# Optimization experiments

Hardware: AMD Instinct MI355X
Metric: run time of the kernel (lower is better)

Reference implementation:

```python
import jax, jax.numpy as jnp
import numpy as np

B, CIN, COUT, T, K = 8, 64, 64, 16384, 127


def setup_inputs() -> dict:
    key = jax.random.key(0)
    kx, kw = jax.random.split(key)
    x = jax.random.normal(kx, (B, CIN, T), dtype=jnp.float32)
    sigma = np.sqrt(2.0 / (CIN * K + COUT)).astype(np.float32)
    W = jax.random.normal(kw, (COUT, CIN, K), dtype=jnp.float32) * sigma
    return {"x": x, "W": W}


def reference(x, W):
    # Full linear convolution via FFT (true convolution, matches
    # torchaudio.functional.fftconvolve), summed over in_channels,
    # then trimmed to mode='same' (output length == T, centered).
    T_ = x.shape[-1]
    K_ = W.shape[-1]
    n = T_ + K_ - 1  # linear-conv length, no circular wraparound
    Xf = jnp.fft.rfft(x, n=n)   # [B, Cin, nf] complex
    Wf = jnp.fft.rfft(W, n=n)   # [Cout, Cin, nf] complex
    # Batched complex multiply-accumulate over in_channels (single pass,
    # no per-output-channel redundant FFTs).
    Yf = jnp.einsum('bif,oif->bof', Xf, Wf)  # [B, Cout, nf]
    y_full = jnp.fft.irfft(Yf, n=n)          # [B, Cout, T+K-1]
    start = (K_ - 1) // 2                    # 'same': centered crop
    return y_full[..., start:start + T_]
```

## Files before the change

kernel.cpp:

```cpp
#include <hip/hip_runtime.h>

#define T_LEN 16384
#define CIN   64
#define COUT  64
#define KTAPS 127
#define TN    512
#define XROWS 640
#define XPITCH_B 144
#define WT_KS 4096

typedef __attribute__((ext_vector_type(8)))  __bf16 bf16x8;
typedef __attribute__((ext_vector_type(16))) float  f32x16;
typedef __attribute__((ext_vector_type(4)))  float  float4v;

__device__ inline unsigned short f2bf(float f) {
    unsigned u = __builtin_bit_cast(unsigned, f);
    u += 0x7fffu + ((u >> 16) & 1u);
    return (unsigned short)(u >> 16);
}

__global__ void wt_transform(const float* __restrict__ W,
                             unsigned short* __restrict__ Wt) {
    int t  = blockIdx.x * 256 + threadIdx.x;
    int kp = t >> 9, c = t & 511;
    int f = c >> 6, kg = (c >> 5) & 1, l31 = c & 31;
    int cc = f >> 1, m = f & 1;
    int o = m * 32 + l31, ib = cc * 16 + kg * 8;
    const float* src = W + (o * CIN + ib) * KTAPS + (126 - kp);
    unsigned short tmp[8];
    #pragma unroll
    for (int e = 0; e < 8; ++e)
        tmp[e] = f2bf(src[e * KTAPS]);
    uint4 pk;
    pk.x = (unsigned)tmp[0] | ((unsigned)tmp[1] << 16);
    pk.y = (unsigned)tmp[2] | ((unsigned)tmp[3] << 16);
    pk.z = (unsigned)tmp[4] | ((unsigned)tmp[5] << 16);
    pk.w = (unsigned)tmp[6] | ((unsigned)tmp[7] << 16);
    *(uint4*)(Wt + kp * WT_KS + c * 8) = pk;
}

__global__ __launch_bounds__(512, 2)
void conv_mfma(const float* __restrict__ x,
               const unsigned short* __restrict__ Wt,
               float* __restrict__ y) {
    __shared__ __align__(16) char pool[XROWS * XPITCH_B];
    unsigned short* xs = (unsigned short*)pool;

    const int tid = threadIdx.x;
    const int bb  = blockIdx.x >> 5;
    const int tt  = blockIdx.x & 31;
    const int t0  = tt * TN;

    {
        const int cin = tid >> 3;
        const int s   = tid & 7;
        const float* xrow = x + (bb * CIN + cin) * T_LEN;
        for (int j = 0; j < 20; ++j) {
            const int w = 32 * j + 4 * s;
            const int u = t0 - 64 + w;
            float4v v;
            if (u >= 0 && u + 4 <= T_LEN) {
                v = *(const float4v*)(xrow + u);
            } else {
                v.x = (u + 0 >= 0 && u + 0 < T_LEN) ? xrow[u + 0] : 0.f;
                v.y = (u + 1 >= 0 && u + 1 < T_LEN) ? xrow[u + 1] : 0.f;
                v.z = (u + 2 >= 0 && u + 2 < T_LEN) ? xrow[u + 2] : 0.f;
                v.w = (u + 3 >= 0 && u + 3 < T_LEN) ? xrow[u + 3] : 0.f;
            }
            #pragma unroll
            for (int e = 0; e < 4; ++e) {
                const int we = w + e;
                const float fv = (e == 0) ? v.x : (e == 1) ? v.y : (e == 2) ? v.z : v.w;
                xs[we * 72 + cin] = f2bf(fv);
            }
        }
    }

    const int lane   = tid & 63;
    const int wv     = tid >> 6;
    const int quad   = wv >> 2;
    const int ww     = wv & 3;
    const int l31    = lane & 31;
    const int kg     = lane >> 5;
    const int twbase = ww * 128;
    const int brow0  = twbase + l31 + 1;

    const int kp0  = quad ? 64 : 0;
    const int ntap = quad ? 63 : 64;

    const char* ab = (const char*)Wt + lane * 16;

    f32x16 acc[2][4] = {};
    uint4 a0r[8], a1r[8];
    uint4 bA[4], bB[4];

    #define LOADA(dst, kp)                                                  \
        do { const char* p_ = ab + (kp) * 8192;                             \
            _Pragma("unroll")                                               \
            for (int f = 0; f < 8; ++f)                                     \
                dst[f] = *(const uint4*)(p_ + f * 1024); } while (0)

    #define LOADB(dst, rb, cidx)                                            \
        do { const char* xp_ = (const char*)xs + (rb) * XPITCH_B            \
                               + ((2 * (cidx) + kg) << 4);                  \
            _Pragma("unroll")                                               \
            for (int n = 0; n < 4; ++n)                                     \
                dst[n] = *(const uint4*)(xp_ + n * (32 * XPITCH_B));        \
        } while (0)

    #define MFMAB(bv, ar, cidx)                                             \
        do { bf16x8 a0 = __builtin_bit_cast(bf16x8, ar[(cidx) * 2 + 0]);    \
            bf16x8 a1 = __builtin_bit_cast(bf16x8, ar[(cidx) * 2 + 1]);     \
            __builtin_amdgcn_s_setprio(1);                                  \
            _Pragma("unroll")                                               \
            for (int n = 0; n < 4; ++n) {                                   \
                bf16x8 b = __builtin_bit_cast(bf16x8, bv[n]);               \
                acc[0][n] = __builtin_amdgcn_mfma_f32_32x32x16_bf16(a0, b, acc[0][n], 0, 0, 0); \
                acc[1][n] = __builtin_amdgcn_mfma_f32_32x32x16_bf16(a1, b, acc[1][n], 0, 0, 0); \
            }                                                               \
            __builtin_amdgcn_s_setprio(0); } while (0)

    #define TAP(ar, kp)                                                     \
        do {                                                                \
            LOADB(bB, brow0 + (kp), 1);     MFMAB(bA, ar, 0);               \
            LOADB(bA, brow0 + (kp), 2);     MFMAB(bB, ar, 1);               \
            LOADB(bB, brow0 + (kp), 3);     MFMAB(bA, ar, 2);               \
            LOADB(bA, brow0 + (kp) + 1, 0); MFMAB(bB, ar, 3);               \
        } while (0)

    LOADA(a0r, kp0);
    __syncthreads();
    LOADB(bA, brow0 + kp0, 0);

    for (int i = 0; i < ntap; i += 2) {
        if (i + 1 < ntap) LOADA(a1r, kp0 + i + 1);
        TAP(a0r, kp0 + i);
        if (i + 2 < ntap) LOADA(a0r, kp0 + i + 2);
        if (i + 1 < ntap) TAP(a1r, kp0 + i + 1);
    }

    __syncthreads();
    float* msm = (float*)pool;
    #pragma unroll
    for (int m = 0; m < 2; ++m) {
        if (quad == 1) {
            #pragma unroll
            for (int n = 0; n < 4; ++n)
                #pragma unroll
                for (int r = 0; r < 16; ++r)
                    msm[(n * 16 + r) * 256 + ww * 64 + lane] = acc[m][n][r];
        }
        __syncthreads();
        if (quad == 0) {
            #pragma unroll
            for (int n = 0; n < 4; ++n)
                #pragma unroll
                for (int r = 0; r < 16; ++r)
                    acc[m][n][r] += msm[(n * 16 + r) * 256 + ww * 64 + lane];
        }
        __syncthreads();
    }

    if (quad == 0) {
        const int ybase = (bb * COUT) * T_LEN;
        #pragma unroll
        for (int m = 0; m < 2; ++m) {
            #pragma unroll
            for (int n = 0; n < 4; ++n) {
                const int t = t0 + twbase + n * 32 + l31;
                #pragma unroll
                for (int r = 0; r < 16; ++r) {
                    const int o = m * 32 + (r & 3) + 8 * (r >> 2) + 4 * kg;
                    y[ybase + o * T_LEN + t] = acc[m][n][r];
                }
            }
        }
    }
}

extern "C" void kernel_launch(void* const* d_in, const int* in_sizes, int n_in,
                              void* d_out, int out_size, void* d_ws, size_t ws_size,
                              hipStream_t stream) {
    const float* x = (const float*)d_in[0];
    const float* W = (const float*)d_in[1];
    float* yout = (float*)d_out;
    unsigned short* Wt = (unsigned short*)d_ws;

    wt_transform<<<(KTAPS * 512) / 256, 256, 0, stream>>>(W, Wt);

    const int grid = 8 * (T_LEN / TN);
    conv_mfma<<<grid, 512, 0, stream>>>(x, Wt, yout);
}
```

Baseline: 118.2 us.

## Double block to 1024 threads with smaller per-wave tiles and streamed A loads

The convolution block grows from 8 to 16 waves, and each wave now covers 64 time columns instead of 128, so it holds a 2x2 accumulator tile instead of 2x4. Weight fragments are no longer kept per tap in 16 registers. Each channel chunk now loads them from global memory just in time and double-buffers them together with the LDS B fragments. The aim is to cut register pressure and raise the number of waves in flight, hiding latency at the cost of more global weight loads per MFMA and less reuse of each A fragment.

Measured after the change: 131.4 us. 11.1% more time.

```diff
diff --git a/kernel.cpp b/kernel.cpp
--- a/kernel.cpp
+++ b/kernel.cpp
@@ -39,7 +39,7 @@
     *(uint4*)(Wt + kp * WT_KS + c * 8) = pk;
 }
 
-__global__ __launch_bounds__(512, 2)
+__global__ __launch_bounds__(1024, 4)
 void conv_mfma(const float* __restrict__ x,
                const unsigned short* __restrict__ Wt,
                float* __restrict__ y) {
@@ -52,11 +52,11 @@
     const int t0  = tt * TN;
 
     {
-        const int cin = tid >> 3;
-        const int s   = tid & 7;
+        const int cin = tid >> 4;
+        const int s   = tid & 15;
         const float* xrow = x + (bb * CIN + cin) * T_LEN;
-        for (int j = 0; j < 20; ++j) {
-            const int w = 32 * j + 4 * s;
+        for (int j = 0; j < 10; ++j) {
+            const int w = 64 * j + 4 * s;
             const int u = t0 - 64 + w;
             float4v v;
             if (u >= 0 && u + 4 <= T_LEN) {
@@ -78,11 +78,11 @@
 
     const int lane   = tid & 63;
     const int wv     = tid >> 6;
-    const int quad   = wv >> 2;
-    const int ww     = wv & 3;
+    const int quad   = wv >> 3;
+    const int ww     = wv & 7;
     const int l31    = lane & 31;
     const int kg     = lane >> 5;
-    const int twbase = ww * 128;
+    const int twbase = ww * 64;
     const int brow0  = twbase + l31 + 1;
 
     const int kp0  = quad ? 64 : 0;
@@ -90,53 +90,43 @@
 
     const char* ab = (const char*)Wt + lane * 16;
 
-    f32x16 acc[2][4] = {};
-    uint4 a0r[8], a1r[8];
-    uint4 bA[4], bB[4];
+    f32x16 acc[2][2] = {};
+    uint4 aC0, aC1, aN0, aN1;
+    uint4 bC0, bC1, bN0, bN1;
 
-    #define LOADA(dst, kp)                                                  \
-        do { const char* p_ = ab + (kp) * 8192;                             \
-            _Pragma("unroll")                                               \
-            for (int f = 0; f < 8; ++f)                                     \
-                dst[f] = *(const uint4*)(p_ + f * 1024); } while (0)
+    #define LOADA2(d0, d1, kp, cc)                                          \
+        do { const char* p_ = ab + (kp) * 8192 + (cc) * 2048;               \
+            d0 = *(const uint4*)(p_);                                       \
+            d1 = *(const uint4*)(p_ + 1024); } while (0)
 
-    #define LOADB(dst, rb, cidx)                                            \
+    #define LOADB2(d0, d1, rb, cc)                                          \
         do { const char* xp_ = (const char*)xs + (rb) * XPITCH_B            \
-                               + ((2 * (cidx) + kg) << 4);                  \
-            _Pragma("unroll")                                               \
-            for (int n = 0; n < 4; ++n)                                     \
-                dst[n] = *(const uint4*)(xp_ + n * (32 * XPITCH_B));        \
+                               + ((2 * (cc) + kg) << 4);                    \
+            d0 = *(const uint4*)(xp_);                                      \
+            d1 = *(const uint4*)(xp_ + 32 * XPITCH_B); } while (0)
+
+    #define MM4(a0v, a1v, b0v, b1v)                                         \
+        do { bf16x8 a0_ = __builtin_bit_cast(bf16x8, a0v);                  \
+            bf16x8 a1_ = __builtin_bit_cast(bf16x8, a1v);                   \
+            bf16x8 b0_ = __builtin_bit_cast(bf16x8, b0v);                   \
+            bf16x8 b1_ = __builtin_bit_cast(bf16x8, b1v);                   \
+            acc[0][0] = __builtin_amdgcn_mfma_f32_32x32x16_bf16(a0_, b0_, acc[0][0], 0, 0, 0); \
+            acc[0][1] = __builtin_amdgcn_mfma_f32_32x32x16_bf16(a0_, b1_, acc[0][1], 0, 0, 0); \
+            acc[1][0] = __builtin_amdgcn_mfma_f32_32x32x16_bf16(a1_, b0_, acc[1][0], 0, 0, 0); \
+            acc[1][1] = __builtin_amdgcn_mfma_f32_32x32x16_bf16(a1_, b1_, acc[1][1], 0, 0, 0); \
         } while (0)
 
-    #define MFMAB(bv, ar, cidx)                                             \
-        do { bf16x8 a0 = __builtin_bit_cast(bf16x8, ar[(cidx) * 2 + 0]);    \
-            bf16x8 a1 = __builtin_bit_cast(bf16x8, ar[(cidx) * 2 + 1]);     \
-            __builtin_amdgcn_s_setprio(1);                                  \
-            _Pragma("unroll")                                               \
-            for (int n = 0; n < 4; ++n) {                                   \
-                bf16x8 b = __builtin_bit_cast(bf16x8, bv[n]);               \
-                acc[0][n] = __builtin_amdgcn_mfma_f32_32x32x16_bf16(a0, b, acc[0][n], 0, 0, 0); \
-                acc[1][n] = __builtin_amdgcn_mfma_f32_32x32x16_bf16(a1, b, acc[1][n], 0, 0, 0); \
-            }                                                               \
-            __builtin_amdgcn_s_setprio(0); } while (0)
+    LOADA2(aC0, aC1, kp0, 0);
+    __syncthreads();
+    LOADB2(bC0, bC1, brow0 + kp0, 0);
 
-    #define TAP(ar, kp)                                                     \
-        do {                                                                \
-            LOADB(bB, brow0 + (kp), 1);     MFMAB(bA, ar, 0);               \
-            LOADB(bA, brow0 + (kp), 2);     MFMAB(bB, ar, 1);               \
-            LOADB(bB, brow0 + (kp), 3);     MFMAB(bA, ar, 2);               \
-            LOADB(bA, brow0 + (kp) + 1, 0); MFMAB(bB, ar, 3);               \
-        } while (0)
-
-    LOADA(a0r, kp0);
-    __syncthreads();
-    LOADB(bA, brow0 + kp0, 0);
-
-    for (int i = 0; i < ntap; i += 2) {
-        if (i + 1 < ntap) LOADA(a1r, kp0 + i + 1);
-        TAP(a0r, kp0 + i);
-        if (i + 2 < ntap) LOADA(a0r, kp0 + i + 2);
-        if (i + 1 < ntap) TAP(a1r, kp0 + i + 1);
+    for (int kp = kp0; kp < kp0 + ntap; ++kp) {
+        const int rb  = brow0 + kp;
+        const int kpn = (kp + 1 < KTAPS) ? kp + 1 : KTAPS - 1;
+        LOADA2(aN0, aN1, kp, 1);  LOADB2(bN0, bN1, rb, 1);  MM4(aC0, aC1, bC0, bC1);
+        LOADA2(aC0, aC1, kp, 2);  LOADB2(bC0, bC1, rb, 2);  MM4(aN0, aN1, bN0, bN1);
+        LOADA2(aN0, aN1, kp, 3);  LOADB2(bN0, bN1, rb, 3);  MM4(aC0, aC1, bC0, bC1);
+        LOADA2(aC0, aC1, kpn, 0); LOADB2(bC0, bC1, rb + 1, 0); MM4(aN0, aN1, bN0, bN1);
     }
 
     __syncthreads();
@@ -145,18 +135,18 @@
     for (int m = 0; m < 2; ++m) {
         if (quad == 1) {
             #pragma unroll
-            for (int n = 0; n < 4; ++n)
+            for (int n = 0; n < 2; ++n)
                 #pragma unroll
                 for (int r = 0; r < 16; ++r)
-                    msm[(n * 16 + r) * 256 + ww * 64 + lane] = acc[m][n][r];
+                    msm[(n * 16 + r) * 512 + ww * 64 + lane] = acc[m][n][r];
         }
         __syncthreads();
         if (quad == 0) {
             #pragma unroll
-            for (int n = 0; n < 4; ++n)
+            for (int n = 0; n < 2; ++n)
                 #pragma unroll
                 for (int r = 0; r < 16; ++r)
-                    acc[m][n][r] += msm[(n * 16 + r) * 256 + ww * 64 + lane];
+                    acc[m][n][r] += msm[(n * 16 + r) * 512 + ww * 64 + lane];
         }
         __syncthreads();
     }
@@ -166,7 +156,7 @@
         #pragma unroll
         for (int m = 0; m < 2; ++m) {
             #pragma unroll
-            for (int n = 0; n < 4; ++n) {
+            for (int n = 0; n < 2; ++n) {
                 const int t = t0 + twbase + n * 32 + l31;
                 #pragma unroll
                 for (int r = 0; r < 16; ++r) {
@@ -189,5 +179,5 @@
     wt_transform<<<(KTAPS * 512) / 256, 256, 0, stream>>>(W, Wt);
 
     const int grid = 8 * (T_LEN / TN);
-    conv_mfma<<<grid, 512, 0, stream>>>(x, Wt, yout);
+    conv_mfma<<<grid, 1024, 0, stream>>>(x, Wt, yout);
 }
```
